# Kernel optimization log

Measured on AMD Instinct MI355X. Metric: run time of the kernel, lower is better.

The kernel has to match this reference:

```python
import jax, jax.numpy as jnp
import numpy as np

B, C, H, W = 8, 512, 64, 64
K = 19       # num classes (Cityscapes)
CT = 256     # transform channels


def _proj(x, w, g, b):
    # 1x1 conv (no bias) + folded eval-mode BatchNorm (per-channel scale g, bias b) + ReLU
    # x: [B,Cin,H,W], w: [Cout,Cin]
    y = jnp.einsum('bchw,oc->bohw', x, w)
    return jax.nn.relu(y * g[None, :, None, None] + b[None, :, None, None])


def setup_inputs() -> dict:
    key = jax.random.key(0)
    ks = jax.random.split(key, 12)
    s = lambda i, shape: jax.random.normal(ks[i], shape, jnp.float32) * 0.05
    ones = lambda n: jnp.ones((n,), jnp.float32)
    zeros = lambda n: jnp.zeros((n,), jnp.float32)
    return {
        'x': jax.random.normal(ks[0], (B, C, H, W), jnp.float32),
        'preds': jax.random.normal(ks[1], (B, K, H, W), jnp.float32),
        'feats_il': jax.random.normal(ks[2], (B, C, H, W), jnp.float32),
        # query_project: two 1x1 conv+BN+ReLU blocks
        'q_w1': s(3, (CT, C)), 'q_g1': ones(CT), 'q_b1': zeros(CT),
        'q_w2': s(4, (CT, CT)), 'q_g2': ones(CT), 'q_b2': zeros(CT),
        # key_project: two 1x1 conv+BN+ReLU blocks
        'k_w1': s(5, (CT, C)), 'k_g1': ones(CT), 'k_b1': zeros(CT),
        'k_w2': s(6, (CT, CT)), 'k_g2': ones(CT), 'k_b2': zeros(CT),
        # value_project: one 1x1 conv+BN+ReLU (value_out_norm=True)
        'v_w': s(7, (CT, C)), 'v_g': ones(CT), 'v_b': zeros(CT),
        # out_project: one 1x1 conv+BN+ReLU
        'o_w': s(8, (C, CT)), 'o_g': ones(C), 'o_b': zeros(C),
    }


def reference(x, preds, feats_il, q_w1, q_g1, q_b1, q_w2, q_g2, q_b2,
              k_w1, k_g1, k_b1, k_w2, k_g2, k_b2, v_w, v_g, v_b, o_w, o_g, o_b):
    b, c, h, w = x.shape
    k = preds.shape[1]
    hw = h * w
    feats = x.reshape(b, c, hw).transpose(0, 2, 1)        # [B,HW,C]
    logits = preds.reshape(b, k, hw).transpose(0, 2, 1)   # [B,HW,K]
    argmax = jnp.argmax(logits, axis=-1)                  # [B,HW]
    onehot = jax.nn.one_hot(argmax, k, dtype=x.dtype)     # [B,HW,K]
    NEG = jnp.asarray(-1e9, x.dtype)
    masked = jnp.where(onehot > 0, logits, NEG)
    # per-class softmax over the pixels assigned to that class
    wgt = jax.nn.softmax(masked, axis=1)                  # [B,HW,K]
    cls_feat = jnp.einsum('bpk,bpc->bkc', wgt, feats)     # [B,K,C]
    # scatter class descriptor back to every pixel of that class
    feats_sl = jnp.take_along_axis(cls_feat, argmax[:, :, None], axis=1)  # [B,HW,C]
    feats_sl = feats_sl.transpose(0, 2, 1).reshape(b, c, h, w)
    # SelfAttentionBlock: query from inputs, key/value from feats_sl
    q = _proj(_proj(x, q_w1, q_g1, q_b1), q_w2, q_g2, q_b2)
    kk = _proj(_proj(feats_sl, k_w1, k_g1, k_b1), k_w2, k_g2, k_b2)
    v = _proj(feats_sl, v_w, v_g, v_b)
    ct = q.shape[1]
    qf = q.reshape(b, ct, hw).transpose(0, 2, 1)          # [B,HW,CT]
    kf = kk.reshape(b, ct, hw)                            # [B,CT,HW]
    vf = v.reshape(b, ct, hw).transpose(0, 2, 1)          # [B,HW,CT]
    sim = jnp.einsum('bqc,bck->bqk', qf, kf) * (ct ** -0.5)
    attn = jax.nn.softmax(sim, axis=-1)
    ctx = jnp.einsum('bqk,bkc->bqc', attn, vf)            # [B,HW,CT]
    ctx = ctx.transpose(0, 2, 1).reshape(b, ct, h, w)
    return _proj(ctx, o_w, o_g, o_b)
```

## Files before the change

kernel.cpp:

```cpp
#include <hip/hip_runtime.h>
#include <math.h>

#define HW 4096
#define NB 8
#define NK 19
#define CIN 512
#define CTC 256

typedef __attribute__((ext_vector_type(8))) short short8;
typedef __attribute__((ext_vector_type(4))) float f32x4;

__device__ inline unsigned short f2bf(float x) {
  unsigned u = __float_as_uint(x);
  return (unsigned short)((u + 0x7fffu + ((u >> 16) & 1u)) >> 16);
}
__device__ inline float bf2f(unsigned short h) {
  return __uint_as_float(((unsigned)h) << 16);
}
__device__ inline void gload16(const void* g, void* l) {
  __builtin_amdgcn_global_load_lds(
      (const __attribute__((address_space(1))) void*)g,
      (__attribute__((address_space(3))) void*)l, 16, 0, 0);
}

__global__ __launch_bounds__(256) void wconv(
    const float* __restrict__ w1, const float* __restrict__ w2,
    const float* __restrict__ wo, unsigned short* __restrict__ wb1,
    unsigned short* __restrict__ wb2, unsigned short* __restrict__ wbo,
    uint4* __restrict__ wgtP_z, uint4* __restrict__ cls_feat_z,
    uint4* __restrict__ atom_z) {
  int gid = blockIdx.x * 256 + threadIdx.x;
  int i = gid * 4;
  const float* src;
  unsigned short* dst;
  int off;
  if (i < 131072) { src = w1; dst = wb1; off = i; }
  else if (i < 196608) { src = w2; dst = wb2; off = i - 131072; }
  else { src = wo; dst = wbo; off = i - 196608; }
  float4 v = *(const float4*)(src + off);
  dst[off + 0] = f2bf(v.x);
  dst[off + 1] = f2bf(v.y);
  dst[off + 2] = f2bf(v.z);
  dst[off + 3] = f2bf(v.w);
  uint4 z = {0u, 0u, 0u, 0u};
  for (int j = gid; j < 131072; j += 81920) wgtP_z[j] = z;
  for (int j = gid; j < 19456; j += 81920) cls_feat_z[j] = z;
  if (gid < 192) atom_z[gid] = z;
}

__global__ __launch_bounds__(256) void k1a(
    const float* __restrict__ preds, float* __restrict__ bestg,
    int* __restrict__ clsg, unsigned int* __restrict__ Mu_g,
    unsigned int* __restrict__ cnt_g) {
  int b = blockIdx.y;
  int p = blockIdx.x * 256 + threadIdx.x;
  __shared__ unsigned int Mw[NK];
  __shared__ unsigned int Cw[NK];
  int tid = threadIdx.x;
  if (tid < NK) { Mw[tid] = 0u; Cw[tid] = 0u; }
  __syncthreads();
  const float* pb = preds + (size_t)b * NK * HW;
  float best = pb[p];
  int bi = 0;
#pragma unroll
  for (int k = 1; k < NK; ++k) {
    float v = pb[k * HW + p];
    if (v > best) { best = v; bi = k; }
  }
  bestg[b * HW + p] = best;
  clsg[b * HW + p] = bi;
  unsigned fb = __float_as_uint(best);
  unsigned key = (fb & 0x80000000u) ? ~fb : (fb | 0x80000000u);
  atomicMax(&Mw[bi], key);
  atomicAdd(&Cw[bi], 1u);
  __syncthreads();
  if (tid < NK) {
    if (Mw[tid]) atomicMax(&Mu_g[b * 32 + tid], Mw[tid]);
    if (Cw[tid]) atomicAdd(&cnt_g[b * 32 + tid], Cw[tid]);
  }
}

__global__ __launch_bounds__(256) void k1b(
    float* __restrict__ bestg, const int* __restrict__ clsg,
    const unsigned int* __restrict__ Mu_g, float* __restrict__ Zf_g) {
  int b = blockIdx.y;
  int p = blockIdx.x * 256 + threadIdx.x;
  __shared__ float Mf[NK];
  __shared__ float Zw[NK];
  int tid = threadIdx.x;
  if (tid < NK) {
    unsigned key = Mu_g[b * 32 + tid];
    float m = -1e30f;
    if (key) {
      unsigned fb = (key & 0x80000000u) ? (key & 0x7fffffffu) : ~key;
      m = __uint_as_float(fb);
    }
    Mf[tid] = m;
    Zw[tid] = 0.f;
  }
  __syncthreads();
  int c = clsg[b * HW + p];
  float e = expf(bestg[b * HW + p] - Mf[c]);
  bestg[b * HW + p] = e;
  atomicAdd(&Zw[c], e);
  __syncthreads();
  if (tid < NK && Zw[tid] != 0.f) atomicAdd(&Zf_g[b * 32 + tid], Zw[tid]);
}

__global__ __launch_bounds__(256) void k1c(
    const float* __restrict__ eg, const int* __restrict__ clsg,
    const float* __restrict__ Zf_g, const unsigned int* __restrict__ cnt_g,
    unsigned short* __restrict__ wgtP, float* __restrict__ countf) {
  int b = blockIdx.y;
  int p = blockIdx.x * 256 + threadIdx.x;
  __shared__ float Zl[NK];
  int tid = threadIdx.x;
  if (tid < NK) Zl[tid] = Zf_g[b * 32 + tid];
  __syncthreads();
  int c = clsg[b * HW + p];
  wgtP[((size_t)b * 32 + c) * HW + p] = f2bf(eg[b * HW + p] / Zl[c]);
  if (blockIdx.x == 0 && tid < NK)
    countf[b * NK + tid] = (float)cnt_g[b * 32 + tid];
}

__global__ __launch_bounds__(256) void xk2(
    const float* __restrict__ x, const unsigned short* __restrict__ wgtP,
    unsigned short* __restrict__ xT, float* __restrict__ cls_feat) {
  __shared__ float tile[64][65];
  __shared__ unsigned short Bs[32 * 516];
  int b = blockIdx.z, c0 = blockIdx.y * 64, pbase = blockIdx.x * 512;
  int tid = threadIdx.x;
  int l = tid & 63, w = tid >> 6;
  {
    const unsigned short* wb =
        wgtP + ((size_t)b * 32 + (tid >> 3)) * HW + pbase;
    int cof = (tid & 7) * 8;
#pragma unroll
    for (int it = 0; it < 8; ++it)
      *(short8*)&Bs[(tid >> 3) * 516 + cof + it * 64] =
          *(const short8*)&wb[cof + it * 64];
  }
  f32x4 acc[2];
  acc[0] = (f32x4){0.f, 0.f, 0.f, 0.f};
  acc[1] = (f32x4){0.f, 0.f, 0.f, 0.f};
  int cbase = w * 16;
  for (int s = 0; s < 8; ++s) {
    int ps = pbase + s * 64;
    __syncthreads();
#pragma unroll
    for (int r = 0; r < 4; ++r) {
      int cl = r * 16 + (tid >> 4);
      int pl = (tid & 15) * 4;
      float4 v = *(const float4*)&x[((size_t)b * CIN + c0 + cl) * HW + ps + pl];
      tile[cl][pl + 0] = v.x;
      tile[cl][pl + 1] = v.y;
      tile[cl][pl + 2] = v.z;
      tile[cl][pl + 3] = v.w;
    }
    __syncthreads();
#pragma unroll
    for (int j = 0; j < 16; ++j) {
      int ploc = j * 4 + w;
      xT[((size_t)b * HW + ps + ploc) * CIN + c0 + l] = f2bf(tile[l][ploc]);
    }
#pragma unroll
    for (int ch = 0; ch < 2; ++ch) {
      int pt = ch * 32 + (l >> 4) * 8;
      union { short8 v; unsigned short u[8]; } af;
      const float* tp = &tile[cbase + (l & 15)][pt];
#pragma unroll
      for (int j = 0; j < 8; ++j) af.u[j] = f2bf(tp[j]);
      int pg = s * 64 + pt;
#pragma unroll
      for (int mf = 0; mf < 2; ++mf) {
        short8 bf = *(const short8*)&Bs[(mf * 16 + (l & 15)) * 516 + pg];
        acc[mf] =
            __builtin_amdgcn_mfma_f32_16x16x32_bf16(af.v, bf, acc[mf], 0, 0, 0);
      }
    }
  }
#pragma unroll
  for (int mf = 0; mf < 2; ++mf) {
    int k = mf * 16 + (l & 15);
    if (k < NK) {
#pragma unroll
      for (int r = 0; r < 4; ++r) {
        int c = c0 + cbase + (l >> 4) * 4 + r;
        atomicAdd(&cls_feat[((size_t)b * NK + k) * CIN + c], acc[mf][r]);
      }
    }
  }
}

__global__ __launch_bounds__(256) void k3a(
    const float* __restrict__ cls_feat, const float* __restrict__ kw1,
    const float* __restrict__ kg1, const float* __restrict__ kb1,
    const float* __restrict__ vw, const float* __restrict__ vg,
    const float* __restrict__ vb, float* __restrict__ h1g,
    float* __restrict__ Vcls) {
  int bk = blockIdx.y;
  int b = bk / NK, kc = bk % NK;
  int q = blockIdx.x;
  __shared__ float cf[CIN];
  int tid = threadIdx.x;
  const float* row = cls_feat + (size_t)bk * CIN;
  for (int i = tid; i < CIN; i += 256) cf[i] = row[i];
  __syncthreads();
  int o = tid >> 1, half = tid & 1;
  int col = q * 64 + (o & 63);
  const float* w =
      (o < 64) ? &kw1[(size_t)col * CIN] : &vw[(size_t)col * CIN];
  int base = half * 256;
  float acc[4] = {0.f, 0.f, 0.f, 0.f};
#pragma unroll 8
  for (int i = 0; i < 64; ++i) {
    float4 w4 = *(const float4*)&w[base + i * 4];
    const float* c4 = &cf[base + i * 4];
    acc[i & 3] += w4.x * c4[0] + w4.y * c4[1] + w4.z * c4[2] + w4.w * c4[3];
  }
  float s = (acc[0] + acc[1]) + (acc[2] + acc[3]);
  s += __shfl_xor(s, 1);
  if (half == 0) {
    if (o < 64) {
      h1g[(size_t)bk * CTC + col] = fmaxf(s * kg1[col] + kb1[col], 0.f);
    } else {
      Vcls[((size_t)b * CTC + col) * NK + kc] =
          fmaxf(s * vg[col] + vb[col], 0.f);
    }
  }
}

__global__ __launch_bounds__(256) void k3b(
    const float* __restrict__ h1g, const float* __restrict__ kw2,
    const float* __restrict__ kg2, const float* __restrict__ kb2,
    unsigned short* __restrict__ KclsT) {
  int bk = blockIdx.y;
  int q = blockIdx.x;
  __shared__ float h1[CTC];
  int tid = threadIdx.x;
  const float* row = h1g + (size_t)bk * CTC;
  if (tid < CTC) h1[tid] = row[tid];
  __syncthreads();
  int o = tid >> 2, part = tid & 3;
  int col = q * 64 + o;
  const float* w = &kw2[(size_t)col * CTC + part * 64];
  const float* c = &h1[part * 64];
  float acc[4] = {0.f, 0.f, 0.f, 0.f};
#pragma unroll
  for (int i = 0; i < 16; ++i) {
    float4 w4 = *(const float4*)&w[i * 4];
    acc[i & 3] += w4.x * c[i * 4] + w4.y * c[i * 4 + 1] + w4.z * c[i * 4 + 2] +
                  w4.w * c[i * 4 + 3];
  }
  float s = (acc[0] + acc[1]) + (acc[2] + acc[3]);
  s += __shfl_xor(s, 1);
  s += __shfl_xor(s, 2);
  if (part == 0)
    KclsT[(size_t)bk * CTC + col] = f2bf(fmaxf(s * kg2[col] + kb2[col], 0.f));
}

template <int KD>
__global__ __launch_bounds__(256) void gemm_mfma(
    const unsigned short* __restrict__ A, const unsigned short* __restrict__ Wb,
    const float* __restrict__ g, const float* __restrict__ bb,
    void* __restrict__ Y, int M, int outmode) {
  __shared__ __align__(16) unsigned short As[2][128 * 32];
  __shared__ __align__(16) unsigned short Bs[2][128 * 32];
  int b = blockIdx.z;
  int n0 = blockIdx.x * 128;
  int m0 = blockIdx.y * 128;
  int tid = threadIdx.x;
  int l = tid & 63, wid = tid >> 6;
  int wr = wid >> 1, wc = wid & 1;
  const unsigned short* Ab = A + (size_t)b * HW * KD;

  f32x4 acc[4][4];
#pragma unroll
  for (int i = 0; i < 4; ++i)
#pragma unroll
    for (int j = 0; j < 4; ++j) acc[i][j] = (f32x4){0.f, 0.f, 0.f, 0.f};

  const int NT = KD / 32;
  auto STAGE = [&](int buf, int t) {
    int k0 = t * 32;
#pragma unroll
    for (int q = 0; q < 2; ++q) {
      int e = q * 2048 + tid * 8;
      int rl = e >> 5, sl = (e >> 3) & 3;
      gload16(Ab + (size_t)(n0 + rl) * KD + k0 + 8 * (sl ^ ((rl >> 1) & 3)),
              &As[buf][q * 2048 + wid * 512]);
    }
#pragma unroll
    for (int q = 0; q < 2; ++q) {
      int e = q * 2048 + tid * 8;
      int rl = e >> 5, sl = (e >> 3) & 3;
      gload16(Wb + (size_t)(m0 + rl) * KD + k0 + 8 * (sl ^ ((rl >> 1) & 3)),
              &Bs[buf][q * 2048 + wid * 512]);
    }
  };
  STAGE(0, 0);
  for (int t = 0; t < NT; ++t) {
    __syncthreads();
    if (t + 1 < NT) STAGE((t + 1) & 1, t + 1);
    int cur = t & 1;
    short8 af[4], bf[4];
#pragma unroll
    for (int f = 0; f < 4; ++f) {
      int nl = wr * 64 + f * 16 + (l & 15);
      af[f] = *(const short8*)&As[cur][nl * 32 + 8 * ((l >> 4) ^ ((nl >> 1) & 3))];
      int ml = wc * 64 + f * 16 + (l & 15);
      bf[f] = *(const short8*)&Bs[cur][ml * 32 + 8 * ((l >> 4) ^ ((ml >> 1) & 3))];
    }
#pragma unroll
    for (int i = 0; i < 4; ++i)
#pragma unroll
      for (int j = 0; j < 4; ++j)
        acc[i][j] =
            __builtin_amdgcn_mfma_f32_16x16x32_bf16(af[i], bf[j], acc[i][j], 0, 0, 0);
  }
  if (outmode == 0) {
    float* Yf = (float*)Y + (size_t)b * M * HW;
#pragma unroll
    for (int j = 0; j < 4; ++j) {
      int m = m0 + wc * 64 + j * 16 + (l & 15);
      float gm = g[m], bm = bb[m];
#pragma unroll
      for (int i = 0; i < 4; ++i) {
        int n = n0 + wr * 64 + i * 16 + (l >> 4) * 4;
        float4 o;
        o.x = fmaxf(acc[i][j][0] * gm + bm, 0.f);
        o.y = fmaxf(acc[i][j][1] * gm + bm, 0.f);
        o.z = fmaxf(acc[i][j][2] * gm + bm, 0.f);
        o.w = fmaxf(acc[i][j][3] * gm + bm, 0.f);
        *(float4*)&Yf[(size_t)m * HW + n] = o;
      }
    }
  } else {
    unsigned short* Yt = (unsigned short*)Y + (size_t)b * HW * M;
#pragma unroll
    for (int j = 0; j < 4; ++j) {
      int m = m0 + wc * 64 + j * 16 + (l & 15);
      float gm = g[m], bm = bb[m];
#pragma unroll
      for (int i = 0; i < 4; ++i) {
        int n = n0 + wr * 64 + i * 16 + (l >> 4) * 4;
#pragma unroll
        for (int r = 0; r < 4; ++r)
          Yt[(size_t)(n + r) * M + m] = f2bf(fmaxf(acc[i][j][r] * gm + bm, 0.f));
      }
    }
  }
}

__global__ __launch_bounds__(256) void k5_mfma(
    const unsigned short* __restrict__ q2T,
    const unsigned short* __restrict__ KclsT, const float* __restrict__ Vcls,
    const float* __restrict__ countf, unsigned short* __restrict__ ctxT) {
  __shared__ __align__(16) unsigned short Kl2[32 * 32 * 8];
  __shared__ __align__(16) unsigned short Vl2[4 * 256 * 8];
  __shared__ __align__(16) char RC[25088];
  __shared__ float cntl[NK];
  unsigned short* Ql = (unsigned short*)RC;
  float* simT = (float*)RC;
  unsigned short* Pl = (unsigned short*)(RC + 16896);

  int b = blockIdx.y;
  int p0 = blockIdx.x * 128;
  int tid = threadIdx.x;
  int l = tid & 63, w = tid >> 6;
  const unsigned short* qb = q2T + ((size_t)b * HW + p0) * CTC;

  for (int i = tid; i < NK * 32; i += 256) {
    int m = i >> 5, s = i & 31;
    short8 v = *(const short8*)&KclsT[((size_t)b * NK + m) * CTC + s * 8];
    *(short8*)&Kl2[(s * 32 + m) * 8] = v;
  }
  for (int i = tid; i < 4 * 256; i += 256) {
    int s = i >> 8, c = i & 255;
    union { short8 v; unsigned short u[8]; } pk;
    const float* vr = &Vcls[((size_t)b * CTC + c) * NK];
#pragma unroll
    for (int j = 0; j < 8; ++j) {
      int k = s * 8 + j;
      pk.u[j] = (k < NK) ? f2bf(vr[k]) : (unsigned short)0;
    }
    *(short8*)&Vl2[(s * 256 + c) * 8] = pk.v;
  }
  if (tid < NK) cntl[tid] = countf[b * NK + tid];

  auto STAGE_Q = [&](int buf, int t) {
#pragma unroll
    for (int q = 0; q < 2; ++q) {
      int e = q * 2048 + tid * 8;
      int rl = e >> 5, sl = (e >> 3) & 3;
      gload16(qb + (size_t)rl * CTC + t * 32 + 8 * (sl ^ ((rl >> 1) & 3)),
              &Ql[buf * 4096 + q * 2048 + w * 512]);
    }
  };
  f32x4 acc[2][2];
#pragma unroll
  for (int i = 0; i < 2; ++i)
#pragma unroll
    for (int j = 0; j < 2; ++j) acc[i][j] = (f32x4){0.f, 0.f, 0.f, 0.f};
  STAGE_Q(0, 0);
  for (int t = 0; t < 8; ++t) {
    __syncthreads();
    if (t + 1 < 8) STAGE_Q((t + 1) & 1, t + 1);
    int cur = t & 1;
    short8 aq[2], bk[2];
#pragma unroll
    for (int f = 0; f < 2; ++f) {
      int nl = w * 32 + f * 16 + (l & 15);
      aq[f] =
          *(const short8*)&Ql[cur * 4096 + nl * 32 + 8 * ((l >> 4) ^ ((nl >> 1) & 3))];
      int s = t * 4 + (l >> 4);
      int ml = f * 16 + (l & 15);
      bk[f] = *(const short8*)&Kl2[(s * 32 + ml) * 8];
    }
#pragma unroll
    for (int i = 0; i < 2; ++i)
#pragma unroll
      for (int j = 0; j < 2; ++j)
        acc[i][j] =
            __builtin_amdgcn_mfma_f32_16x16x32_bf16(aq[i], bk[j], acc[i][j], 0, 0, 0);
  }
  __syncthreads();
#pragma unroll
  for (int i = 0; i < 2; ++i)
#pragma unroll
    for (int j = 0; j < 2; ++j) {
      int m = j * 16 + (l & 15);
      if (m < NK) {
#pragma unroll
        for (int r = 0; r < 4; ++r) {
          int p = w * 32 + i * 16 + (l >> 4) * 4 + r;
          simT[p * 33 + m] = acc[i][j][r];
        }
      }
    }
  __syncthreads();
  if (tid < 128) {
    float sims[NK];
#pragma unroll
    for (int k = 0; k < NK; ++k) sims[k] = simT[tid * 33 + k] * 0.0625f;
    float m = -1e30f;
#pragma unroll
    for (int k = 0; k < NK; ++k)
      if (cntl[k] > 0.f) m = fmaxf(m, sims[k]);
    float d = 0.f;
#pragma unroll
    for (int k = 0; k < NK; ++k) {
      float e = (cntl[k] > 0.f) ? expf(sims[k] - m) : 0.f;
      sims[k] = cntl[k] * e;
      d += sims[k];
    }
    float inv = 1.f / d;
#pragma unroll
    for (int s = 0; s < 4; ++s) {
      union { short8 v; unsigned short u8[8]; } pk;
#pragma unroll
      for (int j = 0; j < 8; ++j) {
        int k = s * 8 + j;
        pk.u8[j] = (k < NK) ? f2bf(sims[k] * inv) : (unsigned short)0;
      }
      *(short8*)&Pl[(s * 128 + tid) * 8] = pk.v;
    }
  }
  __syncthreads();
  short8 ap[2];
#pragma unroll
  for (int f = 0; f < 2; ++f) {
    int nl = w * 32 + f * 16 + (l & 15);
    ap[f] = *(const short8*)&Pl[((l >> 4) * 128 + nl) * 8];
  }
  unsigned short* cb = ctxT + ((size_t)b * HW + p0) * CTC;
#pragma unroll
  for (int mc = 0; mc < 4; ++mc) {
#pragma unroll
    for (int mf = 0; mf < 4; ++mf) {
      int ml = mc * 64 + mf * 16 + (l & 15);
      short8 bv = *(const short8*)&Vl2[((l >> 4) * 256 + ml) * 8];
#pragma unroll
      for (int nf = 0; nf < 2; ++nf) {
        f32x4 z = {0.f, 0.f, 0.f, 0.f};
        f32x4 o = __builtin_amdgcn_mfma_f32_16x16x32_bf16(ap[nf], bv, z, 0, 0, 0);
#pragma unroll
        for (int r = 0; r < 4; ++r) {
          int p = w * 32 + nf * 16 + (l >> 4) * 4 + r;
          cb[(size_t)p * CTC + ml] = f2bf(o[r]);
        }
      }
    }
  }
}

extern "C" void kernel_launch(void* const* d_in, const int* in_sizes, int n_in,
                              void* d_out, int out_size, void* d_ws, size_t ws_size,
                              hipStream_t stream) {
  const float* x = (const float*)d_in[0];
  const float* preds = (const float*)d_in[1];
  const float* q_w1 = (const float*)d_in[3];
  const float* q_g1 = (const float*)d_in[4];
  const float* q_b1 = (const float*)d_in[5];
  const float* q_w2 = (const float*)d_in[6];
  const float* q_g2 = (const float*)d_in[7];
  const float* q_b2 = (const float*)d_in[8];
  const float* k_w1 = (const float*)d_in[9];
  const float* k_g1 = (const float*)d_in[10];
  const float* k_b1 = (const float*)d_in[11];
  const float* k_w2 = (const float*)d_in[12];
  const float* k_g2 = (const float*)d_in[13];
  const float* k_b2 = (const float*)d_in[14];
  const float* v_w = (const float*)d_in[15];
  const float* v_g = (const float*)d_in[16];
  const float* v_b = (const float*)d_in[17];
  const float* o_w = (const float*)d_in[18];
  const float* o_g = (const float*)d_in[19];
  const float* o_b = (const float*)d_in[20];
  float* out = (float*)d_out;

  char* base = (char*)d_ws;
  unsigned short* xT = (unsigned short*)base;
  unsigned short* q2T = xT;
  unsigned short* q1T = (unsigned short*)(base + 33554432);
  unsigned short* ctxT = q1T;
  char* f32r = base + 50331648;
  unsigned short* wgtP = (unsigned short*)f32r;
  float* countf = (float*)(f32r + 2097152);
  float* cls_feat = (float*)(f32r + 2098176);
  unsigned short* KclsT = (unsigned short*)(f32r + 2409472);
  float* Vcls = (float*)(f32r + 2487296);
  unsigned short* wb1 = (unsigned short*)(f32r + 2642944);
  unsigned short* wb2 = (unsigned short*)(f32r + 2905088);
  unsigned short* wbo = (unsigned short*)(f32r + 3036160);
  float* h1g = (float*)(f32r + 3298304);
  float* bestg = (float*)(f32r + 3453952);
  int* clsg = (int*)(f32r + 3585024);
  unsigned int* Mu_g = (unsigned int*)(f32r + 3716096);
  unsigned int* cnt_g = (unsigned int*)(f32r + 3717120);
  float* Zf_g = (float*)(f32r + 3718144);

  wconv<<<320, 256, 0, stream>>>(q_w1, q_w2, o_w, wb1, wb2, wbo,
                                 (uint4*)wgtP, (uint4*)cls_feat,
                                 (uint4*)Mu_g);
  k1a<<<dim3(16, NB), 256, 0, stream>>>(preds, bestg, clsg, Mu_g, cnt_g);
  k1b<<<dim3(16, NB), 256, 0, stream>>>(bestg, clsg, Mu_g, Zf_g);
  k1c<<<dim3(16, NB), 256, 0, stream>>>(bestg, clsg, Zf_g, cnt_g, wgtP,
                                        countf);
  xk2<<<dim3(8, 8, NB), 256, 0, stream>>>(x, wgtP, xT, cls_feat);
  k3a<<<dim3(4, NB * NK), 256, 0, stream>>>(cls_feat, k_w1, k_g1, k_b1, v_w,
                                            v_g, v_b, h1g, Vcls);
  k3b<<<dim3(4, NB * NK), 256, 0, stream>>>(h1g, k_w2, k_g2, k_b2, KclsT);
  gemm_mfma<CIN><<<dim3(32, 2, NB), 256, 0, stream>>>(xT, wb1, q_g1, q_b1,
                                                      (void*)q1T, CTC, 1);
  gemm_mfma<CTC><<<dim3(32, 2, NB), 256, 0, stream>>>(q1T, wb2, q_g2, q_b2,
                                                      (void*)q2T, CTC, 1);
  k5_mfma<<<dim3(HW / 128, NB), 256, 0, stream>>>(q2T, KclsT, Vcls, countf,
                                                  ctxT);
  gemm_mfma<CTC><<<dim3(32, 4, NB), 256, 0, stream>>>(ctxT, wbo, o_g, o_b,
                                                      (void*)out, CIN, 0);
}
```

Before: 137.2 us.

## Fuse second query projection GEMM into attention kernel via shared-memory q2 tile

The second 1x1 query projection (q1 -> q2 with BN+ReLU) now runs inside the attention kernel. Each block computes its 128-pixel x 256-channel q2 tile with MFMA into a swizzled LDS buffer and feeds it straight into the class-similarity MFMA. This removes one kernel launch and the global write and re-read of q2T. In exchange the kernel uses far more LDS (over 100KB, launch bounds set to one block), holds 32 accumulator vectors per thread, and every block reloads the full W2 weight matrix.

```diff
diff --git a/kernel.cpp b/kernel.cpp
--- a/kernel.cpp
+++ b/kernel.cpp
@@ -352,15 +352,18 @@
   }
 }
 
-__global__ __launch_bounds__(256) void k5_mfma(
-    const unsigned short* __restrict__ q2T,
+__global__ __launch_bounds__(256, 1) void g2k5(
+    const unsigned short* __restrict__ q1T, const unsigned short* __restrict__ W2,
+    const float* __restrict__ g2, const float* __restrict__ b2,
     const unsigned short* __restrict__ KclsT, const float* __restrict__ Vcls,
     const float* __restrict__ countf, unsigned short* __restrict__ ctxT) {
+  __shared__ __align__(16) char RC[49152];
+  __shared__ __align__(16) unsigned short Qf[8][4096];
   __shared__ __align__(16) unsigned short Kl2[32 * 32 * 8];
   __shared__ __align__(16) unsigned short Vl2[4 * 256 * 8];
-  __shared__ __align__(16) char RC[25088];
   __shared__ float cntl[NK];
-  unsigned short* Ql = (unsigned short*)RC;
+  unsigned short* As = (unsigned short*)RC;
+  unsigned short* Bs = (unsigned short*)(RC + 16384);
   float* simT = (float*)RC;
   unsigned short* Pl = (unsigned short*)(RC + 16896);
 
@@ -368,7 +371,7 @@
   int p0 = blockIdx.x * 128;
   int tid = threadIdx.x;
   int l = tid & 63, w = tid >> 6;
-  const unsigned short* qb = q2T + ((size_t)b * HW + p0) * CTC;
+  const unsigned short* q1b = q1T + ((size_t)b * HW + p0) * CTC;
 
   for (int i = tid; i < NK * 32; i += 256) {
     int m = i >> 5, s = i & 31;
@@ -388,31 +391,83 @@
   }
   if (tid < NK) cntl[tid] = countf[b * NK + tid];
 
-  auto STAGE_Q = [&](int buf, int t) {
+  auto STAGE_A = [&](int buf, int t) {
+    int k0 = t * 32;
 #pragma unroll
     for (int q = 0; q < 2; ++q) {
       int e = q * 2048 + tid * 8;
       int rl = e >> 5, sl = (e >> 3) & 3;
-      gload16(qb + (size_t)rl * CTC + t * 32 + 8 * (sl ^ ((rl >> 1) & 3)),
-              &Ql[buf * 4096 + q * 2048 + w * 512]);
+      gload16(q1b + (size_t)rl * CTC + k0 + 8 * (sl ^ ((rl >> 1) & 3)),
+              &As[buf * 4096 + q * 2048 + w * 512]);
     }
   };
-  f32x4 acc[2][2];
+  auto STAGE_B = [&](int buf, int t) {
+    int k0 = t * 32;
+#pragma unroll
+    for (int q = 0; q < 4; ++q) {
+      int e = q * 2048 + tid * 8;
+      int rl = e >> 5, sl = (e >> 3) & 3;
+      gload16(W2 + (size_t)rl * CTC + k0 + 8 * (sl ^ ((rl >> 1) & 3)),
+              &Bs[buf * 8192 + q * 2048 + w * 512]);
+    }
+  };
+  f32x4 acc[2][16];
 #pragma unroll
   for (int i = 0; i < 2; ++i)
 #pragma unroll
-    for (int j = 0; j < 2; ++j) acc[i][j] = (f32x4){0.f, 0.f, 0.f, 0.f};
-  STAGE_Q(0, 0);
+    for (int j = 0; j < 16; ++j) acc[i][j] = (f32x4){0.f, 0.f, 0.f, 0.f};
+  STAGE_A(0, 0);
+  STAGE_B(0, 0);
   for (int t = 0; t < 8; ++t) {
     __syncthreads();
-    if (t + 1 < 8) STAGE_Q((t + 1) & 1, t + 1);
+    if (t + 1 < 8) { STAGE_A((t + 1) & 1, t + 1); STAGE_B((t + 1) & 1, t + 1); }
     int cur = t & 1;
-    short8 aq[2], bk[2];
+    short8 af[2];
 #pragma unroll
     for (int f = 0; f < 2; ++f) {
       int nl = w * 32 + f * 16 + (l & 15);
-      aq[f] =
-          *(const short8*)&Ql[cur * 4096 + nl * 32 + 8 * ((l >> 4) ^ ((nl >> 1) & 3))];
+      af[f] =
+          *(const short8*)&As[cur * 4096 + nl * 32 + 8 * ((l >> 4) ^ ((nl >> 1) & 3))];
+    }
+#pragma unroll
+    for (int mf = 0; mf < 16; ++mf) {
+      int ml = mf * 16 + (l & 15);
+      short8 bf =
+          *(const short8*)&Bs[cur * 8192 + ml * 32 + 8 * ((l >> 4) ^ ((ml >> 1) & 3))];
+      acc[0][mf] =
+          __builtin_amdgcn_mfma_f32_16x16x32_bf16(af[0], bf, acc[0][mf], 0, 0, 0);
+      acc[1][mf] =
+          __builtin_amdgcn_mfma_f32_16x16x32_bf16(af[1], bf, acc[1][mf], 0, 0, 0);
+    }
+  }
+#pragma unroll
+  for (int mf = 0; mf < 16; ++mf) {
+    int ch = mf * 16 + (l & 15);
+    float gm = g2[ch], bm = b2[ch];
+    int tq = ch >> 5, slot = (ch >> 3) & 3, wi = ch & 7;
+#pragma unroll
+    for (int i = 0; i < 2; ++i) {
+#pragma unroll
+      for (int r = 0; r < 4; ++r) {
+        int p = w * 32 + i * 16 + (l >> 4) * 4 + r;
+        Qf[tq][p * 32 + 8 * (slot ^ ((p >> 1) & 3)) + wi] =
+            f2bf(fmaxf(acc[i][mf][r] * gm + bm, 0.f));
+      }
+    }
+  }
+  __syncthreads();
+
+  f32x4 a2[2][2];
+#pragma unroll
+  for (int i = 0; i < 2; ++i)
+#pragma unroll
+    for (int j = 0; j < 2; ++j) a2[i][j] = (f32x4){0.f, 0.f, 0.f, 0.f};
+  for (int t = 0; t < 8; ++t) {
+    short8 aq[2], bk[2];
+#pragma unroll
+    for (int f = 0; f < 2; ++f) {
+      int nl = w * 32 + f * 16 + (l & 15);
+      aq[f] = *(const short8*)&Qf[t][nl * 32 + 8 * ((l >> 4) ^ ((nl >> 1) & 3))];
       int s = t * 4 + (l >> 4);
       int ml = f * 16 + (l & 15);
       bk[f] = *(const short8*)&Kl2[(s * 32 + ml) * 8];
@@ -421,8 +476,8 @@
     for (int i = 0; i < 2; ++i)
 #pragma unroll
       for (int j = 0; j < 2; ++j)
-        acc[i][j] =
-            __builtin_amdgcn_mfma_f32_16x16x32_bf16(aq[i], bk[j], acc[i][j], 0, 0, 0);
+        a2[i][j] =
+            __builtin_amdgcn_mfma_f32_16x16x32_bf16(aq[i], bk[j], a2[i][j], 0, 0, 0);
   }
   __syncthreads();
 #pragma unroll
@@ -434,7 +489,7 @@
 #pragma unroll
         for (int r = 0; r < 4; ++r) {
           int p = w * 32 + i * 16 + (l >> 4) * 4 + r;
-          simT[p * 33 + m] = acc[i][j][r];
+          simT[p * 33 + m] = a2[i][j][r];
         }
       }
     }
@@ -521,7 +576,6 @@
 
   char* base = (char*)d_ws;
   unsigned short* xT = (unsigned short*)base;
-  unsigned short* q2T = xT;
   unsigned short* q1T = (unsigned short*)(base + 33554432);
   unsigned short* ctxT = q1T;
   char* f32r = base + 50331648;
@@ -541,8 +595,7 @@
   float* Zf_g = (float*)(f32r + 3718144);
 
   wconv<<<320, 256, 0, stream>>>(q_w1, q_w2, o_w, wb1, wb2, wbo,
-                                 (uint4*)wgtP, (uint4*)cls_feat,
-                                 (uint4*)Mu_g);
+                                 (uint4*)wgtP, (uint4*)cls_feat, (uint4*)Mu_g);
   k1a<<<dim3(16, NB), 256, 0, stream>>>(preds, bestg, clsg, Mu_g, cnt_g);
   k1b<<<dim3(16, NB), 256, 0, stream>>>(bestg, clsg, Mu_g, Zf_g);
   k1c<<<dim3(16, NB), 256, 0, stream>>>(bestg, clsg, Zf_g, cnt_g, wgtP,
@@ -553,10 +606,8 @@
   k3b<<<dim3(4, NB * NK), 256, 0, stream>>>(h1g, k_w2, k_g2, k_b2, KclsT);
   gemm_mfma<CIN><<<dim3(32, 2, NB), 256, 0, stream>>>(xT, wb1, q_g1, q_b1,
                                                       (void*)q1T, CTC, 1);
-  gemm_mfma<CTC><<<dim3(32, 2, NB), 256, 0, stream>>>(q1T, wb2, q_g2, q_b2,
-                                                      (void*)q2T, CTC, 1);
-  k5_mfma<<<dim3(HW / 128, NB), 256, 0, stream>>>(q2T, KclsT, Vcls, countf,
-                                                  ctxT);
+  g2k5<<<dim3(HW / 128, NB), 256, 0, stream>>>(q1T, wb2, q_g2, q_b2, KclsT,
+                                               Vcls, countf, ctxT);
   gemm_mfma<CTC><<<dim3(32, 4, NB), 256, 0, stream>>>(ctxT, wbo, o_g, o_b,
                                                       (void*)out, CIN, 0);
 }
```

New measurement: 132.6 us. 3.3% less time.
